# Kernel tuning notes

Measured on AMD Instinct MI355X. Metric: run time of the kernel, lower is better.

Reference implementation:

```python
import jax, jax.numpy as jnp
import numpy as np

N, E, H, NH = 50000, 800000, 128, 4
D = H // NH
EPS = 1e-5


def _ln(x, g, b):
    m = jnp.mean(x, axis=-1, keepdims=True)
    v = jnp.mean((x - m) ** 2, axis=-1, keepdims=True)
    return (x - m) * jax.lax.rsqrt(v + EPS) * g + b


def setup_inputs() -> dict:
    key = jax.random.key(0)
    ks = jax.random.split(key, 16)

    def lin(k, fi, fo):
        w = jax.random.normal(k, (fi, fo), jnp.float32) * (1.0 / np.sqrt(fi))
        return w, jnp.zeros((fo,), jnp.float32)

    h = jax.random.normal(ks[0], (N, H), jnp.float32)
    e = jax.random.normal(ks[1], (E, H), jnp.float32)
    src = jax.random.randint(ks[2], (E,), 0, N, jnp.int32)
    dst = jax.random.randint(ks[3], (E,), 0, N, jnp.int32)

    Wq, bq = lin(ks[4], H, H)
    Wk, bk = lin(ks[5], 2 * H, H)
    Wv, bv = lin(ks[6], 2 * H, H)
    Wn1, bn1 = lin(ks[7], H, H)
    Wn2, bn2 = lin(ks[8], H, H)
    We1, be1 = lin(ks[9], 3 * H, H)
    We2, be2 = lin(ks[10], H, H)
    gh = jnp.ones((H,), jnp.float32)
    bh = jnp.zeros((H,), jnp.float32)
    ge = jnp.ones((H,), jnp.float32)
    be = jnp.zeros((H,), jnp.float32)

    return dict(h=h, e=e, src=src, dst=dst, Wq=Wq, bq=bq, Wk=Wk, bk=bk,
                Wv=Wv, bv=bv, Wn1=Wn1, bn1=bn1, Wn2=Wn2, bn2=bn2,
                We1=We1, be1=be1, We2=We2, be2=be2, gh=gh, bh=bh, ge=ge, be=be)


def reference(h, e, src, dst, Wq, bq, Wk, bk, Wv, bv, Wn1, bn1, Wn2, bn2,
              We1, be1, We2, be2, gh, bh, ge, be):
    # gather src node features onto edges, concat with edge features: [E, 2H]
    m = jnp.concatenate([h[src], e], axis=-1)
    Q = (h @ Wq + bq).reshape(N, NH, D)
    K = (m @ Wk + bk).reshape(E, NH, D)
    V = (m @ Wv + bv).reshape(E, NH, D)

    # per-edge multihead attention score against destination query: [E, NH]
    s = jnp.sum(Q[dst] * K, axis=-1) / np.sqrt(D).astype(np.float32)

    # destination-grouped (segment) softmax per head
    smax = jax.ops.segment_max(s, dst, num_segments=N)  # [N, NH]
    a = jnp.exp(s - smax[dst])
    denom = jax.ops.segment_sum(a, dst, num_segments=N)  # [N, NH]
    a = a / denom[dst]

    # weighted scatter-sum of values back to destination nodes
    msg = V * a[..., None]  # [E, NH, D]
    h_agg = jax.ops.segment_sum(msg, dst, num_segments=N).reshape(N, H)

    # node MLP update (dropout = identity in eval) + residual + LayerNorm
    h_new = jax.nn.relu(jax.nn.relu(h_agg @ Wn1 + bn1) @ Wn2 + bn2)
    h_out = _ln(h + h_new, gh, bh)

    # edge MLP update on [src_h, dst_h, e] + residual + LayerNorm
    me = jnp.concatenate([h_out[src], h_out[dst], e], axis=-1)  # [E, 3H]
    e_new = jax.nn.relu(jax.nn.relu(me @ We1 + be1) @ We2 + be2)
    e_out = _ln(e + e_new, ge, be)
    return h_out, e_out
```

## Files before the change

### kernel.cpp

```cpp
#include <hip/hip_runtime.h>
#include <hip/hip_bf16.h>

#define NN 50000
#define EE 800000
#define HH 128

typedef __attribute__((ext_vector_type(8))) short bf16x8;
typedef __attribute__((ext_vector_type(4))) float f32x4;

__device__ inline unsigned short f2bf(float f) {
    union { float f; unsigned u; } v; v.f = f;
    unsigned r = v.u + 0x7FFF + ((v.u >> 16) & 1);
    return (unsigned short)(r >> 16);
}

__global__ __launch_bounds__(256) void hist_k(const int* __restrict__ dst, int* __restrict__ cnt) {
    int i = blockIdx.x * 256 + threadIdx.x;
    if (i < EE) atomicAdd(&cnt[dst[i]], 1);
}

__global__ __launch_bounds__(256) void blocksum_k(const int* __restrict__ cnt, int* __restrict__ bsum) {
    __shared__ int sm[256];
    int i = blockIdx.x * 256 + threadIdx.x;
    sm[threadIdx.x] = (i < NN) ? cnt[i] : 0;
    __syncthreads();
    for (int s = 128; s > 0; s >>= 1) {
        if (threadIdx.x < s) sm[threadIdx.x] += sm[threadIdx.x + s];
        __syncthreads();
    }
    if (threadIdx.x == 0) bsum[blockIdx.x] = sm[0];
}

__global__ __launch_bounds__(256) void scanb_k(int* __restrict__ bsum, int nb) {
    __shared__ int sm[256];
    int t = threadIdx.x;
    sm[t] = (t < nb) ? bsum[t] : 0;
    __syncthreads();
    for (int d = 1; d < 256; d <<= 1) {
        int v = (t >= d) ? sm[t - d] : 0;
        __syncthreads();
        sm[t] += v;
        __syncthreads();
    }
    if (t < nb) bsum[t] = sm[t];
}

__global__ __launch_bounds__(256) void offsets_k(const int* __restrict__ cnt, const int* __restrict__ bsum,
                                                 int* __restrict__ offsets, int* __restrict__ cursor) {
    __shared__ int sm[256];
    int b = blockIdx.x, t = threadIdx.x;
    int i = b * 256 + t;
    int c = (i < NN) ? cnt[i] : 0;
    sm[t] = c;
    __syncthreads();
    for (int d = 1; d < 256; d <<= 1) {
        int v = (t >= d) ? sm[t - d] : 0;
        __syncthreads();
        sm[t] += v;
        __syncthreads();
    }
    int incl = sm[t];
    int base = (b == 0) ? 0 : bsum[b - 1];
    int off = base + incl - c;
    if (i < NN) { offsets[i] = off; cursor[i] = off; }
    if (i == NN - 1) offsets[NN] = off + c;
}

__global__ __launch_bounds__(256) void fill_k(const int* __restrict__ dst, int* __restrict__ cursor,
                                              int* __restrict__ eids) {
    int i = blockIdx.x * 256 + threadIdx.x;
    if (i < EE) { int p = atomicAdd(&cursor[dst[i]], 1); eids[p] = i; }
}

__global__ __launch_bounds__(256) void wprep_k(const float* __restrict__ W, unsigned short* __restrict__ out,
                                               int fi, int fo, int n_off, int out_ld) {
    int i = blockIdx.x * 256 + threadIdx.x;
    if (i >= fi * fo) return;
    int n = i / fi, k = i - n * fi;
    out[(size_t)(n_off + n) * out_ld + k] = f2bf(W[(size_t)k * fo + n]);
}

__global__ __launch_bounds__(256) void cvt_k(const float* __restrict__ in, unsigned short* __restrict__ out,
                                             long n8) {
    long i = (long)blockIdx.x * 256 + threadIdx.x;
    if (i >= n8) return;
    const float4* p = (const float4*)in + i * 2;
    float4 a = p[0], b = p[1];
    bf16x8 o = {(short)f2bf(a.x), (short)f2bf(a.y), (short)f2bf(a.z), (short)f2bf(a.w),
                (short)f2bf(b.x), (short)f2bf(b.y), (short)f2bf(b.z), (short)f2bf(b.w)};
    *((bf16x8*)out + i) = o;
}

template <int G, int NCW, int RT, int MODE>
__global__ __launch_bounds__(512, 2) void mm4_k(
    const unsigned short* __restrict__ A0, const int* __restrict__ idx0,
    const unsigned short* __restrict__ A1, const int* __restrict__ idx1,
    const unsigned short* __restrict__ A2, const int* __restrict__ idx2,
    const unsigned short* __restrict__ Wt, const float* __restrict__ bias,
    int M,
    float* __restrict__ Cf, unsigned short* __restrict__ Cb, int out_ld)
{
    constexpr int RW = 8 / NCW;
    constexpr int ROWS = RW * RT * 16;
    constexpr int Ktot = G * 128;
    constexpr int SI = ROWS / 32;
    __shared__ unsigned short Asl[G * ROWS * 128];

    const int t = threadIdx.x;
    const int wid = t >> 6, lane = t & 63;
    const int lr = lane & 15, lk = lane >> 4;
    const int colw = (NCW == 8) ? wid : (wid & 3);
    const int roww = (NCW == 8) ? 0 : (wid >> 2);
    const int col0 = colw << 5;
    const int tbase = blockIdx.x * ROWS;

    const unsigned short* As[3] = {A0, A1, A2};
    const int* igs[3] = {idx0, idx1, idx2};

    #pragma unroll
    for (int g = 0; g < G; ++g) {
        const unsigned short* Ag = As[g];
        const int* ig = igs[g];
        #pragma unroll
        for (int i = 0; i < SI; ++i) {
            int rl = ((i * 8 + wid) << 2) + (lane >> 4);
            int gr = tbase + rl; if (gr >= M) gr = M - 1;
            int rid = ig ? ig[gr] : gr;
            const unsigned short* src = Ag + (size_t)rid * HH + (((lane & 15) ^ (rl & 7)) << 3);
            unsigned short* dst = &Asl[(g * ROWS + ((i * 8 + wid) << 2)) << 7];
            __builtin_amdgcn_global_load_lds((const __attribute__((address_space(1))) void*)src,
                                             (__attribute__((address_space(3))) void*)dst, 16, 0, 0);
        }
    }

    f32x4 acc[RT][2];
    #pragma unroll
    for (int tt = 0; tt < RT; ++tt) { acc[tt][0] = (f32x4){0,0,0,0}; acc[tt][1] = (f32x4){0,0,0,0}; }

    __syncthreads();

    #pragma unroll
    for (int g = 0; g < G; ++g) {
        bf16x8 b[4][2];
        #pragma unroll
        for (int s = 0; s < 4; ++s)
            #pragma unroll
            for (int c = 0; c < 2; ++c)
                b[s][c] = *(const bf16x8*)(Wt + (size_t)(col0 + (c << 4) + lr) * Ktot + (g << 7) + (s << 5) + (lk << 3));

        #pragma unroll
        for (int tt = 0; tt < RT; ++tt) {
            const int tl = (tt * RW + roww) << 4;
            bf16x8 a[4];
            #pragma unroll
            for (int s = 0; s < 4; ++s) {
                const int c16 = ((s << 2) + lk) ^ (lr & 7);
                a[s] = *(const bf16x8*)&Asl[((g * ROWS + tl + lr) << 7) + (c16 << 3)];
            }
            #pragma unroll
            for (int s = 0; s < 4; ++s) {
                acc[tt][0] = __builtin_amdgcn_mfma_f32_16x16x32_bf16(a[s], b[s][0], acc[tt][0], 0, 0, 0);
                acc[tt][1] = __builtin_amdgcn_mfma_f32_16x16x32_bf16(a[s], b[s][1], acc[tt][1], 0, 0, 0);
            }
        }
    }

    float bias2[2] = {bias[col0 + lr], bias[col0 + 16 + lr]};
    #pragma unroll
    for (int tt = 0; tt < RT; ++tt) {
        #pragma unroll
        for (int rr = 0; rr < 4; ++rr) {
            int row = tbase + ((tt * RW + roww) << 4) + (lk << 2) + rr;
            if (row >= M) continue;
            #pragma unroll
            for (int c = 0; c < 2; ++c) {
                float v = acc[tt][c][rr] + bias2[c];
                if (MODE == 1 || MODE == 4) v = fmaxf(v, 0.f);
                size_t o = (size_t)row * out_ld + col0 + (c << 4) + lr;
                if (MODE == 0 || MODE == 1) Cf[o] = v;
                else Cb[o] = f2bf(v);
            }
        }
    }
}

template <int G, int RT>
__global__ __launch_bounds__(512, 2) void mlp_k(
    const unsigned short* __restrict__ A0, const int* __restrict__ idx0,
    const unsigned short* __restrict__ A1, const int* __restrict__ idx1,
    const unsigned short* __restrict__ A2, const int* __restrict__ idx2,
    const unsigned short* __restrict__ W1t, const float* __restrict__ b1,
    const unsigned short* __restrict__ W2t, const float* __restrict__ b2,
    int M,
    float* __restrict__ Cf, unsigned short* __restrict__ Cb2,
    const float* __restrict__ resid, const float* __restrict__ gamma, const float* __restrict__ beta)
{
    constexpr int RW = 2, NCW = 4;
    constexpr int ROWS = RW * RT * 16;
    constexpr int K1 = G * 128;
    constexpr int SI = ROWS / 32;
    __shared__ unsigned short Asl[G * ROWS * 128];
    __shared__ float lnbuf[RT * 32 * 8];

    const int t = threadIdx.x;
    const int wid = t >> 6, lane = t & 63;
    const int lr = lane & 15, lk = lane >> 4;
    const int colw = wid & 3, roww = wid >> 2;
    const int col0 = colw << 5;
    const int tbase = blockIdx.x * ROWS;

    const unsigned short* As[3] = {A0, A1, A2};
    const int* igs[3] = {idx0, idx1, idx2};

    #pragma unroll
    for (int g = 0; g < G; ++g) {
        const unsigned short* Ag = As[g];
        const int* ig = igs[g];
        #pragma unroll
        for (int i = 0; i < SI; ++i) {
            int rl = ((i * 8 + wid) << 2) + (lane >> 4);
            int gr = tbase + rl; if (gr >= M) gr = M - 1;
            int rid = ig ? ig[gr] : gr;
            const unsigned short* src = Ag + (size_t)rid * HH + (((lane & 15) ^ (rl & 7)) << 3);
            unsigned short* dst = &Asl[(g * ROWS + ((i * 8 + wid) << 2)) << 7];
            __builtin_amdgcn_global_load_lds((const __attribute__((address_space(1))) void*)src,
                                             (__attribute__((address_space(3))) void*)dst, 16, 0, 0);
        }
    }

    f32x4 acc[RT][2];
    #pragma unroll
    for (int tt = 0; tt < RT; ++tt) { acc[tt][0] = (f32x4){0,0,0,0}; acc[tt][1] = (f32x4){0,0,0,0}; }

    __syncthreads();

    #pragma unroll
    for (int g = 0; g < G; ++g) {
        bf16x8 b[4][2];
        #pragma unroll
        for (int s = 0; s < 4; ++s)
            #pragma unroll
            for (int c = 0; c < 2; ++c)
                b[s][c] = *(const bf16x8*)(W1t + (size_t)(col0 + (c << 4) + lr) * K1 + (g << 7) + (s << 5) + (lk << 3));

        #pragma unroll
        for (int tt = 0; tt < RT; ++tt) {
            const int tl = (tt * RW + roww) << 4;
            bf16x8 a[4];
            #pragma unroll
            for (int s = 0; s < 4; ++s) {
                const int c16 = ((s << 2) + lk) ^ (lr & 7);
                a[s] = *(const bf16x8*)&Asl[((g * ROWS + tl + lr) << 7) + (c16 << 3)];
            }
            #pragma unroll
            for (int s = 0; s < 4; ++s) {
                acc[tt][0] = __builtin_amdgcn_mfma_f32_16x16x32_bf16(a[s], b[s][0], acc[tt][0], 0, 0, 0);
                acc[tt][1] = __builtin_amdgcn_mfma_f32_16x16x32_bf16(a[s], b[s][1], acc[tt][1], 0, 0, 0);
            }
        }
    }

    __syncthreads();

    {
        float b1c[2] = {b1[col0 + lr], b1[col0 + 16 + lr]};
        #pragma unroll
        for (int tt = 0; tt < RT; ++tt) {
            #pragma unroll
            for (int rr = 0; rr < 4; ++rr) {
                int rowl = ((tt * RW + roww) << 4) + (lk << 2) + rr;
                #pragma unroll
                for (int c = 0; c < 2; ++c) {
                    int col = col0 + (c << 4) + lr;
                    int chunk = (col >> 3) ^ (rowl & 7);
                    Asl[(rowl << 7) + (chunk << 3) + (col & 7)] =
                        f2bf(fmaxf(acc[tt][c][rr] + b1c[c], 0.f));
                }
            }
        }
    }

    __syncthreads();

    f32x4 acc2[RT][2];
    #pragma unroll
    for (int tt = 0; tt < RT; ++tt) { acc2[tt][0] = (f32x4){0,0,0,0}; acc2[tt][1] = (f32x4){0,0,0,0}; }

    {
        bf16x8 b[4][2];
        #pragma unroll
        for (int s = 0; s < 4; ++s)
            #pragma unroll
            for (int c = 0; c < 2; ++c)
                b[s][c] = *(const bf16x8*)(W2t + (size_t)(col0 + (c << 4) + lr) * 128 + (s << 5) + (lk << 3));

        #pragma unroll
        for (int tt = 0; tt < RT; ++tt) {
            const int tl = (tt * RW + roww) << 4;
            bf16x8 a[4];
            #pragma unroll
            for (int s = 0; s < 4; ++s) {
                const int c16 = ((s << 2) + lk) ^ (lr & 7);
                a[s] = *(const bf16x8*)&Asl[((tl + lr) << 7) + (c16 << 3)];
            }
            #pragma unroll
            for (int s = 0; s < 4; ++s) {
                acc2[tt][0] = __builtin_amdgcn_mfma_f32_16x16x32_bf16(a[s], b[s][0], acc2[tt][0], 0, 0, 0);
                acc2[tt][1] = __builtin_amdgcn_mfma_f32_16x16x32_bf16(a[s], b[s][1], acc2[tt][1], 0, 0, 0);
            }
        }
    }

    float b2c[2] = {b2[col0 + lr], b2[col0 + 16 + lr]};
    float g2[2] = {gamma[col0 + lr], gamma[col0 + 16 + lr]};
    float be2[2] = {beta[col0 + lr], beta[col0 + 16 + lr]};

    #pragma unroll
    for (int tt = 0; tt < RT; ++tt) {
        #pragma unroll
        for (int rr = 0; rr < 4; ++rr) {
            int row = tbase + ((tt * RW + roww) << 4) + (lk << 2) + rr;
            int rowc = (row < M) ? row : M - 1;
            float sum = 0.f, sq = 0.f;
            #pragma unroll
            for (int c = 0; c < 2; ++c) {
                float v = fmaxf(acc2[tt][c][rr] + b2c[c], 0.f);
                v += resid[(size_t)rowc * HH + col0 + (c << 4) + lr];
                acc2[tt][c][rr] = v;
                sum += v; sq += v * v;
            }
            sum += __shfl_xor(sum, 1); sq += __shfl_xor(sq, 1);
            sum += __shfl_xor(sum, 2); sq += __shfl_xor(sq, 2);
            sum += __shfl_xor(sum, 4); sq += __shfl_xor(sq, 4);
            sum += __shfl_xor(sum, 8); sq += __shfl_xor(sq, 8);
            if (lr == 0) {
                int rls = (roww << 4) + (lk << 2) + rr;
                lnbuf[((tt * 32 + rls) << 3) + (colw << 1) + 0] = sum;
                lnbuf[((tt * 32 + rls) << 3) + (colw << 1) + 1] = sq;
            }
        }
    }
    __syncthreads();
    #pragma unroll
    for (int tt = 0; tt < RT; ++tt) {
        #pragma unroll
        for (int rr = 0; rr < 4; ++rr) {
            int rls = (roww << 4) + (lk << 2) + rr;
            float s4 = 0.f, q4 = 0.f;
            #pragma unroll
            for (int cw = 0; cw < 4; ++cw) {
                s4 += lnbuf[((tt * 32 + rls) << 3) + (cw << 1) + 0];
                q4 += lnbuf[((tt * 32 + rls) << 3) + (cw << 1) + 1];
            }
            const float mean = s4 * (1.f / 128.f);
            const float var = q4 * (1.f / 128.f) - mean * mean;
            const float rs = rsqrtf(var + 1e-5f);
            int row = tbase + ((tt * RW + roww) << 4) + (lk << 2) + rr;
            if (row < M) {
                #pragma unroll
                for (int c = 0; c < 2; ++c) {
                    float o = (acc2[tt][c][rr] - mean) * rs * g2[c] + be2[c];
                    size_t idx = (size_t)row * HH + col0 + (c << 4) + lr;
                    Cf[idx] = o;
                    if (Cb2) Cb2[idx] = f2bf(o);
                }
            }
        }
    }
}

template <int RT>
__global__ __launch_bounds__(512, 2) void kv_k(
    const unsigned short* __restrict__ hbf, const int* __restrict__ src,
    const unsigned short* __restrict__ ebf,
    const unsigned short* __restrict__ Wt, const float* __restrict__ bias,
    const float* __restrict__ Q, const int* __restrict__ dst,
    int M, unsigned short* __restrict__ V, float* __restrict__ sbuf)
{
    constexpr int ROWS = RT * 16;
    constexpr int Ktot = 256;
    constexpr int SI = ROWS / 32;
    __shared__ unsigned short Asl[2 * ROWS * 128];

    const int t = threadIdx.x;
    const int wid = t >> 6, lane = t & 63;
    const int lr = lane & 15, lk = lane >> 4;
    const int col0 = wid << 5;
    const int tbase = blockIdx.x * ROWS;

    int dstid[RT][4];
    if (wid < 4) {
        #pragma unroll
        for (int tt = 0; tt < RT; ++tt)
            #pragma unroll
            for (int rr = 0; rr < 4; ++rr) {
                int row = tbase + (tt << 4) + (lk << 2) + rr;
                dstid[tt][rr] = dst[(row < M) ? row : M - 1];
            }
    }

    #pragma unroll
    for (int g = 0; g < 2; ++g) {
        const unsigned short* Ag = g ? ebf : hbf;
        #pragma unroll
        for (int i = 0; i < SI; ++i) {
            int rl = ((i * 8 + wid) << 2) + (lane >> 4);
            int gr = tbase + rl; if (gr >= M) gr = M - 1;
            int rid = g ? gr : src[gr];
            const unsigned short* srcp = Ag + (size_t)rid * HH + (((lane & 15) ^ (rl & 7)) << 3);
            unsigned short* dstp = &Asl[(g * ROWS + ((i * 8 + wid) << 2)) << 7];
            __builtin_amdgcn_global_load_lds((const __attribute__((address_space(1))) void*)srcp,
                                             (__attribute__((address_space(3))) void*)dstp, 16, 0, 0);
        }
    }

    f32x4 acc[RT][2];
    #pragma unroll
    for (int tt = 0; tt < RT; ++tt) { acc[tt][0] = (f32x4){0,0,0,0}; acc[tt][1] = (f32x4){0,0,0,0}; }

    __syncthreads();

    #pragma unroll
    for (int g = 0; g < 2; ++g) {
        bf16x8 b[4][2];
        #pragma unroll
        for (int s = 0; s < 4; ++s)
            #pragma unroll
            for (int c = 0; c < 2; ++c)
                b[s][c] = *(const bf16x8*)(Wt + (size_t)(col0 + (c << 4) + lr) * Ktot + (g << 7) + (s << 5) + (lk << 3));

        #pragma unroll
        for (int tt = 0; tt < RT; ++tt) {
            bf16x8 a[4];
            #pragma unroll
            for (int s = 0; s < 4; ++s) {
                const int c16 = ((s << 2) + lk) ^ (lr & 7);
                a[s] = *(const bf16x8*)&Asl[((g * ROWS + (tt << 4) + lr) << 7) + (c16 << 3)];
            }
            #pragma unroll
            for (int s = 0; s < 4; ++s) {
                acc[tt][0] = __builtin_amdgcn_mfma_f32_16x16x32_bf16(a[s], b[s][0], acc[tt][0], 0, 0, 0);
                acc[tt][1] = __builtin_amdgcn_mfma_f32_16x16x32_bf16(a[s], b[s][1], acc[tt][1], 0, 0, 0);
            }
        }
    }

    float bias2[2] = {bias[col0 + lr], bias[col0 + 16 + lr]};

    if (wid < 4) {
        #pragma unroll
        for (int tt = 0; tt < RT; ++tt) {
            #pragma unroll
            for (int rr = 0; rr < 4; ++rr) {
                int row = tbase + (tt << 4) + (lk << 2) + rr;
                int d = dstid[tt][rr];
                float q0 = Q[(size_t)d * HH + col0 + lr];
                float q1 = Q[(size_t)d * HH + col0 + 16 + lr];
                float p = (acc[tt][0][rr] + bias2[0]) * q0 + (acc[tt][1][rr] + bias2[1]) * q1;
                p += __shfl_xor(p, 1); p += __shfl_xor(p, 2);
                p += __shfl_xor(p, 4); p += __shfl_xor(p, 8);
                if (lr == 0 && row < M)
                    sbuf[(size_t)row * 4 + wid] = p * 0.17677669529663687f;
            }
        }
    } else {
        #pragma unroll
        for (int tt = 0; tt < RT; ++tt) {
            #pragma unroll
            for (int rr = 0; rr < 4; ++rr) {
                int row = tbase + (tt << 4) + (lk << 2) + rr;
                if (row >= M) continue;
                #pragma unroll
                for (int c = 0; c < 2; ++c)
                    V[(size_t)row * HH + (col0 - 128) + (c << 4) + lr] = f2bf(acc[tt][c][rr] + bias2[c]);
            }
        }
    }
}

__global__ __launch_bounds__(256) void agg_k(const __hip_bfloat16* __restrict__ Vb,
                                             const float* __restrict__ s,
                                             const int* __restrict__ offsets,
                                             const int* __restrict__ eids,
                                             unsigned short* __restrict__ hagg)
{
    const int t = threadIdx.x;
    const int n = blockIdx.x * 4 + (t >> 6);
    if (n >= NN) return;
    const int lane = t & 63;
    const int c0 = lane, c1 = lane + 64;
    const int h0 = lane >> 5, h1 = h0 + 2;
    const int o0 = offsets[n], o1 = offsets[n + 1];
    float m0 = -1e30f, m1 = -1e30f, d0 = 0.f, d1 = 0.f, a0 = 0.f, a1 = 0.f;
    for (int j = o0; j < o1; ++j) {
        const int e = eids[j];
        const float s0 = s[(size_t)e * 4 + h0];
        const float s1 = s[(size_t)e * 4 + h1];
        const float v0 = __bfloat162float(Vb[(size_t)e * HH + c0]);
        const float v1 = __bfloat162float(Vb[(size_t)e * HH + c1]);
        float nm = fmaxf(m0, s0);
        float sc = __expf(m0 - nm);
        float w  = __expf(s0 - nm);
        d0 = d0 * sc + w; a0 = a0 * sc + w * v0; m0 = nm;
        nm = fmaxf(m1, s1);
        sc = __expf(m1 - nm);
        w  = __expf(s1 - nm);
        d1 = d1 * sc + w; a1 = a1 * sc + w * v1; m1 = nm;
    }
    const bool any = (o1 > o0);
    hagg[(size_t)n * HH + c0] = any ? f2bf(a0 / d0) : 0;
    hagg[(size_t)n * HH + c1] = any ? f2bf(a1 / d1) : 0;
}

extern "C" void kernel_launch(void* const* d_in, const int* in_sizes, int n_in,
                              void* d_out, int out_size, void* d_ws, size_t ws_size,
                              hipStream_t stream)
{
    const float* h   = (const float*)d_in[0];
    const float* e   = (const float*)d_in[1];
    const int*   src = (const int*)d_in[2];
    const int*   dst = (const int*)d_in[3];
    const float* Wq  = (const float*)d_in[4];
    const float* bq  = (const float*)d_in[5];
    const float* Wk  = (const float*)d_in[6];
    const float* bk  = (const float*)d_in[7];
    const float* Wv  = (const float*)d_in[8];
    const float* bv  = (const float*)d_in[9];
    const float* Wn1 = (const float*)d_in[10];
    const float* bn1 = (const float*)d_in[11];
    const float* Wn2 = (const float*)d_in[12];
    const float* bn2 = (const float*)d_in[13];
    const float* We1 = (const float*)d_in[14];
    const float* be1 = (const float*)d_in[15];
    const float* We2 = (const float*)d_in[16];
    const float* be2 = (const float*)d_in[17];
    const float* gh  = (const float*)d_in[18];
    const float* bh  = (const float*)d_in[19];
    const float* ge  = (const float*)d_in[20];
    const float* be_ = (const float*)d_in[21];
    (void)in_sizes; (void)n_in; (void)out_size; (void)ws_size;

    float* h_out = (float*)d_out;
    float* e_out = (float*)d_out + (size_t)NN * HH;

    char* ws = (char*)d_ws;
    size_t off = 0;
    auto carve = [&](size_t bytes) { void* p = ws + off; off += (bytes + 255) & ~(size_t)255; return p; };
    unsigned short* Vbuf = (unsigned short*)carve((size_t)EE * HH * 2);
    unsigned short* ebf = (unsigned short*)carve((size_t)EE * HH * 2);
    float* Q      = (float*)carve((size_t)NN * HH * 4);
    float* sbuf   = (float*)carve((size_t)EE * 4 * 4);
    unsigned short* hagg = (unsigned short*)carve((size_t)NN * HH * 2);
    unsigned short* hobf = (unsigned short*)carve((size_t)NN * HH * 2);
    unsigned short* hbf  = (unsigned short*)carve((size_t)NN * HH * 2);
    int* cursor   = (int*)carve((size_t)NN * 4);
    int* offsets  = (int*)carve((size_t)(NN + 1) * 4);
    int* bsum     = (int*)carve(256 * 4);
    int* eids     = (int*)carve((size_t)EE * 4);
    unsigned short* Wq_s  = (unsigned short*)carve(128 * 128 * 2);
    unsigned short* Wkv_s = (unsigned short*)carve(256 * 256 * 2);
    unsigned short* Wn1_s = (unsigned short*)carve(128 * 128 * 2);
    unsigned short* Wn2_s = (unsigned short*)carve(128 * 128 * 2);
    unsigned short* We1_s = (unsigned short*)carve(128 * 384 * 2);
    unsigned short* We2_s = (unsigned short*)carve(128 * 128 * 2);
    float* b_kv   = (float*)carve(256 * 4);

    const int nb = (NN + 255) / 256;

    wprep_k<<<(128 * 128 + 255) / 256, 256, 0, stream>>>(Wq,  Wq_s,  128, 128, 0, 128);
    wprep_k<<<(256 * 128 + 255) / 256, 256, 0, stream>>>(Wk,  Wkv_s, 256, 128, 0, 256);
    wprep_k<<<(256 * 128 + 255) / 256, 256, 0, stream>>>(Wv,  Wkv_s, 256, 128, 128, 256);
    wprep_k<<<(128 * 128 + 255) / 256, 256, 0, stream>>>(Wn1, Wn1_s, 128, 128, 0, 128);
    wprep_k<<<(128 * 128 + 255) / 256, 256, 0, stream>>>(Wn2, Wn2_s, 128, 128, 0, 128);
    wprep_k<<<(384 * 128 + 255) / 256, 256, 0, stream>>>(We1, We1_s, 384, 128, 0, 384);
    wprep_k<<<(128 * 128 + 255) / 256, 256, 0, stream>>>(We2, We2_s, 128, 128, 0, 128);
    hipMemcpyAsync(b_kv,       bk, 128 * 4, hipMemcpyDeviceToDevice, stream);
    hipMemcpyAsync(b_kv + 128, bv, 128 * 4, hipMemcpyDeviceToDevice, stream);

    cvt_k<<<(NN * HH / 8 + 255) / 256, 256, 0, stream>>>(h, hbf, (long)NN * HH / 8);
    cvt_k<<<(EE * HH / 8 + 255) / 256, 256, 0, stream>>>(e, ebf, (long)EE * HH / 8);

    hipMemsetAsync(cursor, 0, (size_t)NN * 4, stream);
    hist_k<<<(EE + 255) / 256, 256, 0, stream>>>(dst, cursor);
    blocksum_k<<<nb, 256, 0, stream>>>(cursor, bsum);
    scanb_k<<<1, 256, 0, stream>>>(bsum, nb);
    offsets_k<<<nb, 256, 0, stream>>>(cursor, bsum, offsets, cursor);
    fill_k<<<(EE + 255) / 256, 256, 0, stream>>>(dst, cursor, eids);

    mm4_k<1, 4, 4, 0><<<(NN + 127) / 128, 512, 0, stream>>>(
        hbf, nullptr, nullptr, nullptr, nullptr, nullptr,
        Wq_s, bq, NN, Q, nullptr, 128);

    kv_k<4><<<EE / 64, 512, 0, stream>>>(
        hbf, src, ebf, Wkv_s, b_kv, Q, dst, EE, Vbuf, sbuf);

    agg_k<<<(NN + 3) / 4, 256, 0, stream>>>((const __hip_bfloat16*)Vbuf, sbuf, offsets, eids, hagg);

    mlp_k<1, 4><<<(NN + 127) / 128, 512, 0, stream>>>(
        hagg, nullptr, nullptr, nullptr, nullptr, nullptr,
        Wn1_s, bn1, Wn2_s, bn2, NN, h_out, hobf, h, gh, bh);

    mlp_k<3, 2><<<EE / 64, 512, 0, stream>>>(
        hobf, src, hobf, dst, ebf, nullptr,
        We1_s, be1, We2_s, be2, EE, e_out, nullptr, e, ge, be_);
}
```

Measured before the change: 1.340 ms.

## Make edge GEMM kernels persistent with double-buffered async LDS staging

Replaces the one-tile-per-block KV projection and MLP kernels with multi-tile loops that prefetch the next tile's gathered rows into a second LDS buffer while computing the current tile. Waits use explicit vmcnt and lgkmcnt counts, and residual loads are hoisted before the compute. The MLP tile shrinks to 32 rows with a separate intermediate buffer. The goal is to hide gather latency behind MFMA work, at the cost of fragile hand-set wait counts and fewer blocks in flight.

```diff
diff --git a/kernel.cpp b/kernel.cpp
--- a/kernel.cpp
+++ b/kernel.cpp
@@ -13,6 +13,19 @@
     unsigned r = v.u + 0x7FFF + ((v.u >> 16) & 1);
     return (unsigned short)(r >> 16);
 }
+
+template <int N> __device__ __forceinline__ void wait_vmcnt() {
+    static_assert(N == 4 || N == 9 || N == 11, "");
+    if constexpr (N == 4)  asm volatile("s_waitcnt vmcnt(4)" ::: "memory");
+    if constexpr (N == 9)  asm volatile("s_waitcnt vmcnt(9)" ::: "memory");
+    if constexpr (N == 11) asm volatile("s_waitcnt vmcnt(11)" ::: "memory");
+    __builtin_amdgcn_sched_barrier(0);
+}
+__device__ __forceinline__ void wait_lgkm0() {
+    asm volatile("s_waitcnt lgkmcnt(0)" ::: "memory");
+    __builtin_amdgcn_sched_barrier(0);
+}
+__device__ __forceinline__ void membar() { asm volatile("" ::: "memory"); }
 
 __global__ __launch_bounds__(256) void hist_k(const int* __restrict__ dst, int* __restrict__ cnt) {
     int i = blockIdx.x * 256 + threadIdx.x;
@@ -94,8 +107,6 @@
 template <int G, int NCW, int RT, int MODE>
 __global__ __launch_bounds__(512, 2) void mm4_k(
     const unsigned short* __restrict__ A0, const int* __restrict__ idx0,
-    const unsigned short* __restrict__ A1, const int* __restrict__ idx1,
-    const unsigned short* __restrict__ A2, const int* __restrict__ idx2,
     const unsigned short* __restrict__ Wt, const float* __restrict__ bias,
     int M,
     float* __restrict__ Cf, unsigned short* __restrict__ Cb, int out_ld)
@@ -109,24 +120,19 @@
     const int t = threadIdx.x;
     const int wid = t >> 6, lane = t & 63;
     const int lr = lane & 15, lk = lane >> 4;
-    const int colw = (NCW == 8) ? wid : (wid & 3);
-    const int roww = (NCW == 8) ? 0 : (wid >> 2);
+    const int colw = wid & 3;
+    const int roww = wid >> 2;
     const int col0 = colw << 5;
     const int tbase = blockIdx.x * ROWS;
 
-    const unsigned short* As[3] = {A0, A1, A2};
-    const int* igs[3] = {idx0, idx1, idx2};
-
     #pragma unroll
     for (int g = 0; g < G; ++g) {
-        const unsigned short* Ag = As[g];
-        const int* ig = igs[g];
         #pragma unroll
         for (int i = 0; i < SI; ++i) {
             int rl = ((i * 8 + wid) << 2) + (lane >> 4);
             int gr = tbase + rl; if (gr >= M) gr = M - 1;
-            int rid = ig ? ig[gr] : gr;
-            const unsigned short* src = Ag + (size_t)rid * HH + (((lane & 15) ^ (rl & 7)) << 3);
+            int rid = idx0 ? idx0[gr] : gr;
+            const unsigned short* src = A0 + (size_t)rid * HH + (((lane & 15) ^ (rl & 7)) << 3);
             unsigned short* dst = &Asl[(g * ROWS + ((i * 8 + wid) << 2)) << 7];
             __builtin_amdgcn_global_load_lds((const __attribute__((address_space(1))) void*)src,
                                              (__attribute__((address_space(3))) void*)dst, 16, 0, 0);
@@ -175,7 +181,7 @@
             #pragma unroll
             for (int c = 0; c < 2; ++c) {
                 float v = acc[tt][c][rr] + bias2[c];
-                if (MODE == 1 || MODE == 4) v = fmaxf(v, 0.f);
+                if (MODE == 1) v = fmaxf(v, 0.f);
                 size_t o = (size_t)row * out_ld + col0 + (c << 4) + lr;
                 if (MODE == 0 || MODE == 1) Cf[o] = v;
                 else Cb[o] = f2bf(v);
@@ -184,149 +190,263 @@
     }
 }
 
-template <int G, int RT>
-__global__ __launch_bounds__(512, 2) void mlp_k(
+template <int TPB>
+__global__ __launch_bounds__(512, 2) void kvp_k(
+    const unsigned short* __restrict__ hbf, const int* __restrict__ src,
+    const unsigned short* __restrict__ ebf,
+    const unsigned short* __restrict__ Wt, const float* __restrict__ bias,
+    const float* __restrict__ Q, const int* __restrict__ dst,
+    int M, int ntiles, unsigned short* __restrict__ V, float* __restrict__ sbuf)
+{
+    __shared__ unsigned short Abuf[2][2 * 64 * 128];
+
+    const int t = threadIdx.x;
+    const int wid = t >> 6, lane = t & 63;
+    const int lr = lane & 15, lk = lane >> 4;
+    const int col0 = wid << 5;
+    const int tb = blockIdx.x * TPB;
+
+    auto stage = [&](int tile, int buf) {
+        const int base = tile * 64;
+        #pragma unroll
+        for (int g = 0; g < 2; ++g) {
+            const unsigned short* Ag = g ? ebf : hbf;
+            #pragma unroll
+            for (int i = 0; i < 2; ++i) {
+                int rl = i * 32 + (t >> 4);
+                int gr = base + rl; if (gr >= M) gr = M - 1;
+                int rid = g ? gr : src[gr];
+                const unsigned short* sp = Ag + (size_t)rid * HH + (((t & 15) ^ (rl & 7)) << 3);
+                unsigned short* dp = &Abuf[buf][((g * 64 + rl) << 7) + ((t & 15) << 3)];
+                __builtin_amdgcn_global_load_lds((const __attribute__((address_space(1))) void*)sp,
+                                                 (__attribute__((address_space(3))) void*)dp, 16, 0, 0);
+            }
+        }
+    };
+
+    float bias2[2] = {bias[col0 + lr], bias[col0 + 16 + lr]};
+
+    stage(min(tb, ntiles - 1), 0);
+
+    for (int tt = 0; tt < TPB; ++tt) {
+        const int cur = tt & 1;
+        const int tile = min(tb + tt, ntiles - 1);
+        const int rbase = tile * 64;
+
+        if (tt + 1 < TPB) stage(min(tb + tt + 1, ntiles - 1), cur ^ 1);
+
+        int dstid[4][4];
+        if (wid < 4) {
+            #pragma unroll
+            for (int t4 = 0; t4 < 4; ++t4)
+                #pragma unroll
+                for (int rr = 0; rr < 4; ++rr) {
+                    int row = rbase + (t4 << 4) + (lk << 2) + rr;
+                    dstid[t4][rr] = dst[(row < M) ? row : M - 1];
+                }
+        }
+
+        wait_vmcnt<4>();
+        __builtin_amdgcn_s_barrier();
+
+        f32x4 acc[4][2];
+        #pragma unroll
+        for (int t4 = 0; t4 < 4; ++t4) { acc[t4][0] = (f32x4){0,0,0,0}; acc[t4][1] = (f32x4){0,0,0,0}; }
+
+        #pragma unroll
+        for (int g = 0; g < 2; ++g) {
+            bf16x8 b[4][2];
+            #pragma unroll
+            for (int s = 0; s < 4; ++s)
+                #pragma unroll
+                for (int c = 0; c < 2; ++c)
+                    b[s][c] = *(const bf16x8*)(Wt + (size_t)(col0 + (c << 4) + lr) * 256 + (g << 7) + (s << 5) + (lk << 3));
+
+            #pragma unroll
+            for (int t4 = 0; t4 < 4; ++t4) {
+                bf16x8 a[4];
+                #pragma unroll
+                for (int s = 0; s < 4; ++s) {
+                    const int c16 = ((s << 2) + lk) ^ (lr & 7);
+                    a[s] = *(const bf16x8*)&Abuf[cur][((g * 64 + (t4 << 4) + lr) << 7) + (c16 << 3)];
+                }
+                #pragma unroll
+                for (int s = 0; s < 4; ++s) {
+                    acc[t4][0] = __builtin_amdgcn_mfma_f32_16x16x32_bf16(a[s], b[s][0], acc[t4][0], 0, 0, 0);
+                    acc[t4][1] = __builtin_amdgcn_mfma_f32_16x16x32_bf16(a[s], b[s][1], acc[t4][1], 0, 0, 0);
+                }
+            }
+        }
+
+        if (wid < 4) {
+            #pragma unroll
+            for (int t4 = 0; t4 < 4; ++t4) {
+                #pragma unroll
+                for (int rr = 0; rr < 4; ++rr) {
+                    int row = rbase + (t4 << 4) + (lk << 2) + rr;
+                    int d = dstid[t4][rr];
+                    float q0 = Q[(size_t)d * HH + col0 + lr];
+                    float q1 = Q[(size_t)d * HH + col0 + 16 + lr];
+                    float p = (acc[t4][0][rr] + bias2[0]) * q0 + (acc[t4][1][rr] + bias2[1]) * q1;
+                    p += __shfl_xor(p, 1); p += __shfl_xor(p, 2);
+                    p += __shfl_xor(p, 4); p += __shfl_xor(p, 8);
+                    if (lr == 0 && row < M)
+                        sbuf[(size_t)row * 4 + wid] = p * 0.17677669529663687f;
+                }
+            }
+        } else {
+            #pragma unroll
+            for (int t4 = 0; t4 < 4; ++t4) {
+                #pragma unroll
+                for (int rr = 0; rr < 4; ++rr) {
+                    int row = rbase + (t4 << 4) + (lk << 2) + rr;
+                    if (row >= M) continue;
+                    #pragma unroll
+                    for (int c = 0; c < 2; ++c)
+                        V[(size_t)row * HH + (col0 - 128) + (c << 4) + lr] = f2bf(acc[t4][c][rr] + bias2[c]);
+                }
+            }
+        }
+
+        membar();
+        __builtin_amdgcn_s_barrier();
+    }
+}
+
+template <int G, int TPB>
+__global__ __launch_bounds__(512, 2) void mlpp_k(
     const unsigned short* __restrict__ A0, const int* __restrict__ idx0,
     const unsigned short* __restrict__ A1, const int* __restrict__ idx1,
     const unsigned short* __restrict__ A2, const int* __restrict__ idx2,
     const unsigned short* __restrict__ W1t, const float* __restrict__ b1,
     const unsigned short* __restrict__ W2t, const float* __restrict__ b2,
-    int M,
+    int M, int ntiles,
     float* __restrict__ Cf, unsigned short* __restrict__ Cb2,
     const float* __restrict__ resid, const float* __restrict__ gamma, const float* __restrict__ beta)
 {
-    constexpr int RW = 2, NCW = 4;
-    constexpr int ROWS = RW * RT * 16;
     constexpr int K1 = G * 128;
-    constexpr int SI = ROWS / 32;
-    __shared__ unsigned short Asl[G * ROWS * 128];
-    __shared__ float lnbuf[RT * 32 * 8];
+    __shared__ unsigned short Abuf[2][G * 32 * 128];
+    __shared__ unsigned short tbuf[32 * 128];
+    __shared__ float lnbuf[32 * 8];
 
     const int t = threadIdx.x;
     const int wid = t >> 6, lane = t & 63;
     const int lr = lane & 15, lk = lane >> 4;
-    const int colw = wid & 3, roww = wid >> 2;
-    const int col0 = colw << 5;
-    const int tbase = blockIdx.x * ROWS;
+    const int cw = wid & 3, rg = wid >> 2;
+    const int col0 = cw << 5;
+    const int tb = blockIdx.x * TPB;
 
     const unsigned short* As[3] = {A0, A1, A2};
     const int* igs[3] = {idx0, idx1, idx2};
 
-    #pragma unroll
-    for (int g = 0; g < G; ++g) {
-        const unsigned short* Ag = As[g];
-        const int* ig = igs[g];
-        #pragma unroll
-        for (int i = 0; i < SI; ++i) {
-            int rl = ((i * 8 + wid) << 2) + (lane >> 4);
-            int gr = tbase + rl; if (gr >= M) gr = M - 1;
+    auto stage = [&](int tile, int buf) {
+        const int base = tile * 32;
+        #pragma unroll
+        for (int g = 0; g < G; ++g) {
+            const unsigned short* Ag = As[g];
+            const int* ig = igs[g];
+            int rl = t >> 4;
+            int gr = base + rl; if (gr >= M) gr = M - 1;
             int rid = ig ? ig[gr] : gr;
-            const unsigned short* src = Ag + (size_t)rid * HH + (((lane & 15) ^ (rl & 7)) << 3);
-            unsigned short* dst = &Asl[(g * ROWS + ((i * 8 + wid) << 2)) << 7];
-            __builtin_amdgcn_global_load_lds((const __attribute__((address_space(1))) void*)src,
-                                             (__attribute__((address_space(3))) void*)dst, 16, 0, 0);
-        }
-    }
-
-    f32x4 acc[RT][2];
-    #pragma unroll
-    for (int tt = 0; tt < RT; ++tt) { acc[tt][0] = (f32x4){0,0,0,0}; acc[tt][1] = (f32x4){0,0,0,0}; }
-
-    __syncthreads();
-
-    #pragma unroll
-    for (int g = 0; g < G; ++g) {
-        bf16x8 b[4][2];
-        #pragma unroll
-        for (int s = 0; s < 4; ++s)
+            const unsigned short* sp = Ag + (size_t)rid * HH + (((t & 15) ^ (rl & 7)) << 3);
+            unsigned short* dp = &Abuf[buf][((g * 32 + rl) << 7) + ((t & 15) << 3)];
+            __builtin_amdgcn_global_load_lds((const __attribute__((address_space(1))) void*)sp,
+                                             (__attribute__((address_space(3))) void*)dp, 16, 0, 0);
+        }
+    };
+
+    float b1c[2] = {b1[col0 + lr], b1[col0 + 16 + lr]};
+    float b2c[2] = {b2[col0 + lr], b2[col0 + 16 + lr]};
+    float g2[2]  = {gamma[col0 + lr], gamma[col0 + 16 + lr]};
+    float be2[2] = {beta[col0 + lr], beta[col0 + 16 + lr]};
+
+    stage(min(tb, ntiles - 1), 0);
+
+    for (int tt = 0; tt < TPB; ++tt) {
+        const int cur = tt & 1;
+        const int tile = min(tb + tt, ntiles - 1);
+        const int rbase = tile * 32;
+
+        if (tt + 1 < TPB) stage(min(tb + tt + 1, ntiles - 1), cur ^ 1);
+
+        float rp[4][2];
+        #pragma unroll
+        for (int rr = 0; rr < 4; ++rr) {
+            int row = rbase + (rg << 4) + (lk << 2) + rr;
+            int rowc = (row < M) ? row : M - 1;
             #pragma unroll
             for (int c = 0; c < 2; ++c)
-                b[s][c] = *(const bf16x8*)(W1t + (size_t)(col0 + (c << 4) + lr) * K1 + (g << 7) + (s << 5) + (lk << 3));
-
-        #pragma unroll
-        for (int tt = 0; tt < RT; ++tt) {
-            const int tl = (tt * RW + roww) << 4;
+                rp[rr][c] = resid[(size_t)rowc * HH + col0 + (c << 4) + lr];
+        }
+
+        wait_vmcnt<(G == 3) ? 11 : 9>();
+        __builtin_amdgcn_s_barrier();
+
+        f32x4 acc[2] = {(f32x4){0,0,0,0}, (f32x4){0,0,0,0}};
+        #pragma unroll
+        for (int g = 0; g < G; ++g) {
+            bf16x8 b[4][2];
+            #pragma unroll
+            for (int s = 0; s < 4; ++s)
+                #pragma unroll
+                for (int c = 0; c < 2; ++c)
+                    b[s][c] = *(const bf16x8*)(W1t + (size_t)(col0 + (c << 4) + lr) * K1 + (g << 7) + (s << 5) + (lk << 3));
             bf16x8 a[4];
             #pragma unroll
             for (int s = 0; s < 4; ++s) {
                 const int c16 = ((s << 2) + lk) ^ (lr & 7);
-                a[s] = *(const bf16x8*)&Asl[((g * ROWS + tl + lr) << 7) + (c16 << 3)];
+                a[s] = *(const bf16x8*)&Abuf[cur][((g * 32 + (rg << 4) + lr) << 7) + (c16 << 3)];
             }
             #pragma unroll
             for (int s = 0; s < 4; ++s) {
-                acc[tt][0] = __builtin_amdgcn_mfma_f32_16x16x32_bf16(a[s], b[s][0], acc[tt][0], 0, 0, 0);
-                acc[tt][1] = __builtin_amdgcn_mfma_f32_16x16x32_bf16(a[s], b[s][1], acc[tt][1], 0, 0, 0);
-            }
-        }
-    }
-
-    __syncthreads();
-
-    {
-        float b1c[2] = {b1[col0 + lr], b1[col0 + 16 + lr]};
-        #pragma unroll
-        for (int tt = 0; tt < RT; ++tt) {
-            #pragma unroll
-            for (int rr = 0; rr < 4; ++rr) {
-                int rowl = ((tt * RW + roww) << 4) + (lk << 2) + rr;
-                #pragma unroll
-                for (int c = 0; c < 2; ++c) {
-                    int col = col0 + (c << 4) + lr;
-                    int chunk = (col >> 3) ^ (rowl & 7);
-                    Asl[(rowl << 7) + (chunk << 3) + (col & 7)] =
-                        f2bf(fmaxf(acc[tt][c][rr] + b1c[c], 0.f));
-                }
-            }
-        }
-    }
-
-    __syncthreads();
-
-    f32x4 acc2[RT][2];
-    #pragma unroll
-    for (int tt = 0; tt < RT; ++tt) { acc2[tt][0] = (f32x4){0,0,0,0}; acc2[tt][1] = (f32x4){0,0,0,0}; }
-
-    {
-        bf16x8 b[4][2];
-        #pragma unroll
-        for (int s = 0; s < 4; ++s)
-            #pragma unroll
-            for (int c = 0; c < 2; ++c)
-                b[s][c] = *(const bf16x8*)(W2t + (size_t)(col0 + (c << 4) + lr) * 128 + (s << 5) + (lk << 3));
-
-        #pragma unroll
-        for (int tt = 0; tt < RT; ++tt) {
-            const int tl = (tt * RW + roww) << 4;
+                acc[0] = __builtin_amdgcn_mfma_f32_16x16x32_bf16(a[s], b[s][0], acc[0], 0, 0, 0);
+                acc[1] = __builtin_amdgcn_mfma_f32_16x16x32_bf16(a[s], b[s][1], acc[1], 0, 0, 0);
+            }
+        }
+
+        #pragma unroll
+        for (int rr = 0; rr < 4; ++rr) {
+            int rowl = (rg << 4) + (lk << 2) + rr;
+            #pragma unroll
+            for (int c = 0; c < 2; ++c) {
+                int col = col0 + (c << 4) + lr;
+                int chunk = (col >> 3) ^ (rowl & 7);
+                tbuf[(rowl << 7) + (chunk << 3) + (col & 7)] =
+                    f2bf(fmaxf(acc[c][rr] + b1c[c], 0.f));
+            }
+        }
+        wait_lgkm0();
+        __builtin_amdgcn_s_barrier();
+
+        f32x4 acc2[2] = {(f32x4){0,0,0,0}, (f32x4){0,0,0,0}};
+        {
+            bf16x8 b[4][2];
+            #pragma unroll
+            for (int s = 0; s < 4; ++s)
+                #pragma unroll
+                for (int c = 0; c < 2; ++c)
+                    b[s][c] = *(const bf16x8*)(W2t + (size_t)(col0 + (c << 4) + lr) * 128 + (s << 5) + (lk << 3));
             bf16x8 a[4];
             #pragma unroll
             for (int s = 0; s < 4; ++s) {
                 const int c16 = ((s << 2) + lk) ^ (lr & 7);
-                a[s] = *(const bf16x8*)&Asl[((tl + lr) << 7) + (c16 << 3)];
+                a[s] = *(const bf16x8*)&tbuf[(((rg << 4) + lr) << 7) + (c16 << 3)];
             }
             #pragma unroll
             for (int s = 0; s < 4; ++s) {
-                acc2[tt][0] = __builtin_amdgcn_mfma_f32_16x16x32_bf16(a[s], b[s][0], acc2[tt][0], 0, 0, 0);
-                acc2[tt][1] = __builtin_amdgcn_mfma_f32_16x16x32_bf16(a[s], b[s][1], acc2[tt][1], 0, 0, 0);
-            }
-        }
-    }
-
-    float b2c[2] = {b2[col0 + lr], b2[col0 + 16 + lr]};
-    float g2[2] = {gamma[col0 + lr], gamma[col0 + 16 + lr]};
-    float be2[2] = {beta[col0 + lr], beta[col0 + 16 + lr]};
-
-    #pragma unroll
-    for (int tt = 0; tt < RT; ++tt) {
+                acc2[0] = __builtin_amdgcn_mfma_f32_16x16x32_bf16(a[s], b[s][0], acc2[0], 0, 0, 0);
+                acc2[1] = __builtin_amdgcn_mfma_f32_16x16x32_bf16(a[s], b[s][1], acc2[1], 0, 0, 0);
+            }
+        }
+
+        float xv[4][2];
         #pragma unroll
         for (int rr = 0; rr < 4; ++rr) {
-            int row = tbase + ((tt * RW + roww) << 4) + (lk << 2) + rr;
-            int rowc = (row < M) ? row : M - 1;
             float sum = 0.f, sq = 0.f;
             #pragma unroll
             for (int c = 0; c < 2; ++c) {
-                float v = fmaxf(acc2[tt][c][rr] + b2c[c], 0.f);
-                v += resid[(size_t)rowc * HH + col0 + (c << 4) + lr];
-                acc2[tt][c][rr] = v;
+                float v = fmaxf(acc2[c][rr] + b2c[c], 0.f) + rp[rr][c];
+                xv[rr][c] = v;
                 sum += v; sq += v * v;
             }
             sum += __shfl_xor(sum, 1); sq += __shfl_xor(sq, 1);
@@ -334,145 +454,35 @@
             sum += __shfl_xor(sum, 4); sq += __shfl_xor(sq, 4);
             sum += __shfl_xor(sum, 8); sq += __shfl_xor(sq, 8);
             if (lr == 0) {
-                int rls = (roww << 4) + (lk << 2) + rr;
-                lnbuf[((tt * 32 + rls) << 3) + (colw << 1) + 0] = sum;
-                lnbuf[((tt * 32 + rls) << 3) + (colw << 1) + 1] = sq;
-            }
-        }
-    }
-    __syncthreads();
-    #pragma unroll
-    for (int tt = 0; tt < RT; ++tt) {
+                int rowl = (rg << 4) + (lk << 2) + rr;
+                lnbuf[(rowl << 3) + (cw << 1) + 0] = sum;
+                lnbuf[(rowl << 3) + (cw << 1) + 1] = sq;
+            }
+        }
+        wait_lgkm0();
+        __builtin_amdgcn_s_barrier();
+
         #pragma unroll
         for (int rr = 0; rr < 4; ++rr) {
-            int rls = (roww << 4) + (lk << 2) + rr;
+            int rowl = (rg << 4) + (lk << 2) + rr;
             float s4 = 0.f, q4 = 0.f;
             #pragma unroll
-            for (int cw = 0; cw < 4; ++cw) {
-                s4 += lnbuf[((tt * 32 + rls) << 3) + (cw << 1) + 0];
-                q4 += lnbuf[((tt * 32 + rls) << 3) + (cw << 1) + 1];
+            for (int w4 = 0; w4 < 4; ++w4) {
+                s4 += lnbuf[(rowl << 3) + (w4 << 1) + 0];
+                q4 += lnbuf[(rowl << 3) + (w4 << 1) + 1];
             }
             const float mean = s4 * (1.f / 128.f);
             const float var = q4 * (1.f / 128.f) - mean * mean;
             const float rs = rsqrtf(var + 1e-5f);
-            int row = tbase + ((tt * RW + roww) << 4) + (lk << 2) + rr;
+            int row = rbase + rowl;
             if (row < M) {
                 #pragma unroll
                 for (int c = 0; c < 2; ++c) {
-                    float o = (acc2[tt][c][rr] - mean) * rs * g2[c] + be2[c];
+                    float o = (xv[rr][c] - mean) * rs * g2[c] + be2[c];
                     size_t idx = (size_t)row * HH + col0 + (c << 4) + lr;
                     Cf[idx] = o;
                     if (Cb2) Cb2[idx] = f2bf(o);
                 }
-            }
-        }
-    }
-}
-
-template <int RT>
-__global__ __launch_bounds__(512, 2) void kv_k(
-    const unsigned short* __restrict__ hbf, const int* __restrict__ src,
-    const unsigned short* __restrict__ ebf,
-    const unsigned short* __restrict__ Wt, const float* __restrict__ bias,
-    const float* __restrict__ Q, const int* __restrict__ dst,
-    int M, unsigned short* __restrict__ V, float* __restrict__ sbuf)
-{
-    constexpr int ROWS = RT * 16;
-    constexpr int Ktot = 256;
-    constexpr int SI = ROWS / 32;
-    __shared__ unsigned short Asl[2 * ROWS * 128];
-
-    const int t = threadIdx.x;
-    const int wid = t >> 6, lane = t & 63;
-    const int lr = lane & 15, lk = lane >> 4;
-    const int col0 = wid << 5;
-    const int tbase = blockIdx.x * ROWS;
-
-    int dstid[RT][4];
-    if (wid < 4) {
-        #pragma unroll
-        for (int tt = 0; tt < RT; ++tt)
-            #pragma unroll
-            for (int rr = 0; rr < 4; ++rr) {
-                int row = tbase + (tt << 4) + (lk << 2) + rr;
-                dstid[tt][rr] = dst[(row < M) ? row : M - 1];
-            }
-    }
-
-    #pragma unroll
-    for (int g = 0; g < 2; ++g) {
-        const unsigned short* Ag = g ? ebf : hbf;
-        #pragma unroll
-        for (int i = 0; i < SI; ++i) {
-            int rl = ((i * 8 + wid) << 2) + (lane >> 4);
-            int gr = tbase + rl; if (gr >= M) gr = M - 1;
-            int rid = g ? gr : src[gr];
-            const unsigned short* srcp = Ag + (size_t)rid * HH + (((lane & 15) ^ (rl & 7)) << 3);
-            unsigned short* dstp = &Asl[(g * ROWS + ((i * 8 + wid) << 2)) << 7];
-            __builtin_amdgcn_global_load_lds((const __attribute__((address_space(1))) void*)srcp,
-                                             (__attribute__((address_space(3))) void*)dstp, 16, 0, 0);
-        }
-    }
-
-    f32x4 acc[RT][2];
-    #pragma unroll
-    for (int tt = 0; tt < RT; ++tt) { acc[tt][0] = (f32x4){0,0,0,0}; acc[tt][1] = (f32x4){0,0,0,0}; }
-
-    __syncthreads();
-
-    #pragma unroll
-    for (int g = 0; g < 2; ++g) {
-        bf16x8 b[4][2];
-        #pragma unroll
-        for (int s = 0; s < 4; ++s)
-            #pragma unroll
-            for (int c = 0; c < 2; ++c)
-                b[s][c] = *(const bf16x8*)(Wt + (size_t)(col0 + (c << 4) + lr) * Ktot + (g << 7) + (s << 5) + (lk << 3));
-
-        #pragma unroll
-        for (int tt = 0; tt < RT; ++tt) {
-            bf16x8 a[4];
-            #pragma unroll
-            for (int s = 0; s < 4; ++s) {
-                const int c16 = ((s << 2) + lk) ^ (lr & 7);
-                a[s] = *(const bf16x8*)&Asl[((g * ROWS + (tt << 4) + lr) << 7) + (c16 << 3)];
-            }
-            #pragma unroll
-            for (int s = 0; s < 4; ++s) {
-                acc[tt][0] = __builtin_amdgcn_mfma_f32_16x16x32_bf16(a[s], b[s][0], acc[tt][0], 0, 0, 0);
-                acc[tt][1] = __builtin_amdgcn_mfma_f32_16x16x32_bf16(a[s], b[s][1], acc[tt][1], 0, 0, 0);
-            }
-        }
-    }
-
-    float bias2[2] = {bias[col0 + lr], bias[col0 + 16 + lr]};
-
-    if (wid < 4) {
-        #pragma unroll
-        for (int tt = 0; tt < RT; ++tt) {
-            #pragma unroll
-            for (int rr = 0; rr < 4; ++rr) {
-                int row = tbase + (tt << 4) + (lk << 2) + rr;
-                int d = dstid[tt][rr];
-                float q0 = Q[(size_t)d * HH + col0 + lr];
-                float q1 = Q[(size_t)d * HH + col0 + 16 + lr];
-                float p = (acc[tt][0][rr] + bias2[0]) * q0 + (acc[tt][1][rr] + bias2[1]) * q1;
-                p += __shfl_xor(p, 1); p += __shfl_xor(p, 2);
-                p += __shfl_xor(p, 4); p += __shfl_xor(p, 8);
-                if (lr == 0 && row < M)
-                    sbuf[(size_t)row * 4 + wid] = p * 0.17677669529663687f;
-            }
-        }
-    } else {
-        #pragma unroll
-        for (int tt = 0; tt < RT; ++tt) {
-            #pragma unroll
-            for (int rr = 0; rr < 4; ++rr) {
-                int row = tbase + (tt << 4) + (lk << 2) + rr;
-                if (row >= M) continue;
-                #pragma unroll
-                for (int c = 0; c < 2; ++c)
-                    V[(size_t)row * HH + (col0 - 128) + (c << 4) + lr] = f2bf(acc[tt][c][rr] + bias2[c]);
             }
         }
     }
@@ -588,19 +598,27 @@
     fill_k<<<(EE + 255) / 256, 256, 0, stream>>>(dst, cursor, eids);
 
     mm4_k<1, 4, 4, 0><<<(NN + 127) / 128, 512, 0, stream>>>(
-        hbf, nullptr, nullptr, nullptr, nullptr, nullptr,
-        Wq_s, bq, NN, Q, nullptr, 128);
-
-    kv_k<4><<<EE / 64, 512, 0, stream>>>(
-        hbf, src, ebf, Wkv_s, b_kv, Q, dst, EE, Vbuf, sbuf);
+        hbf, nullptr, Wq_s, bq, NN, Q, nullptr, 128);
+
+    {
+        const int ntiles = EE / 64;
+        kvp_k<10><<<(ntiles + 9) / 10, 512, 0, stream>>>(
+            hbf, src, ebf, Wkv_s, b_kv, Q, dst, EE, ntiles, Vbuf, sbuf);
+    }
 
     agg_k<<<(NN + 3) / 4, 256, 0, stream>>>((const __hip_bfloat16*)Vbuf, sbuf, offsets, eids, hagg);
 
-    mlp_k<1, 4><<<(NN + 127) / 128, 512, 0, stream>>>(
-        hagg, nullptr, nullptr, nullptr, nullptr, nullptr,
-        Wn1_s, bn1, Wn2_s, bn2, NN, h_out, hobf, h, gh, bh);
-
-    mlp_k<3, 2><<<EE / 64, 512, 0, stream>>>(
-        hobf, src, hobf, dst, ebf, nullptr,
-        We1_s, be1, We2_s, be2, EE, e_out, nullptr, e, ge, be_);
-}
+    {
+        const int ntiles = (NN + 31) / 32;
+        mlpp_k<1, 3><<<(ntiles + 2) / 3, 512, 0, stream>>>(
+            hagg, nullptr, nullptr, nullptr, nullptr, nullptr,
+            Wn1_s, bn1, Wn2_s, bn2, NN, ntiles, h_out, hobf, h, gh, bh);
+    }
+
+    {
+        const int ntiles = EE / 32;
+        mlpp_k<3, 10><<<(ntiles + 9) / 10, 512, 0, stream>>>(
+            hobf, src, hobf, dst, ebf, nullptr,
+            We1_s, be1, We2_s, be2, EE, ntiles, e_out, nullptr, e, ge, be_);
+    }
+}
```

Result: slower. 2.049 ms (+52.9%).

## Process edges in destination-sorted order so aggregation reads V and scores contiguously

Applied to the files above, without the earlier changes.

The fill kernel now also writes src and dst indices permuted into CSR (dst-sorted) order. The K/V projection kernel walks edges in that sorted order, gathering e rows through eids and h rows through the permuted src. It writes V and scores at sorted positions, so the aggregation kernel reads them contiguously instead of through eids. This replaces scattered per-edge gathers of V and scores in aggregation with a gather of e rows in the KV kernel, at the cost of two extra int arrays. Unused generality in mm4_k (extra operand slots, NCW==8 path, MODE 4) is also removed.

```diff
diff --git a/kernel.cpp b/kernel.cpp
--- a/kernel.cpp
+++ b/kernel.cpp
@@ -66,10 +66,17 @@
     if (i == NN - 1) offsets[NN] = off + c;
 }
 
-__global__ __launch_bounds__(256) void fill_k(const int* __restrict__ dst, int* __restrict__ cursor,
-                                              int* __restrict__ eids) {
+__global__ __launch_bounds__(256) void fill_k(const int* __restrict__ src, const int* __restrict__ dst,
+                                              int* __restrict__ cursor, int* __restrict__ eids,
+                                              int* __restrict__ srcc, int* __restrict__ dstc) {
     int i = blockIdx.x * 256 + threadIdx.x;
-    if (i < EE) { int p = atomicAdd(&cursor[dst[i]], 1); eids[p] = i; }
+    if (i < EE) {
+        int d = dst[i];
+        int p = atomicAdd(&cursor[d], 1);
+        eids[p] = i;
+        srcc[p] = src[i];
+        dstc[p] = d;
+    }
 }
 
 __global__ __launch_bounds__(256) void wprep_k(const float* __restrict__ W, unsigned short* __restrict__ out,
@@ -94,8 +101,6 @@
 template <int G, int NCW, int RT, int MODE>
 __global__ __launch_bounds__(512, 2) void mm4_k(
     const unsigned short* __restrict__ A0, const int* __restrict__ idx0,
-    const unsigned short* __restrict__ A1, const int* __restrict__ idx1,
-    const unsigned short* __restrict__ A2, const int* __restrict__ idx2,
     const unsigned short* __restrict__ Wt, const float* __restrict__ bias,
     int M,
     float* __restrict__ Cf, unsigned short* __restrict__ Cb, int out_ld)
@@ -109,24 +114,19 @@
     const int t = threadIdx.x;
     const int wid = t >> 6, lane = t & 63;
     const int lr = lane & 15, lk = lane >> 4;
-    const int colw = (NCW == 8) ? wid : (wid & 3);
-    const int roww = (NCW == 8) ? 0 : (wid >> 2);
+    const int colw = wid & 3;
+    const int roww = wid >> 2;
     const int col0 = colw << 5;
     const int tbase = blockIdx.x * ROWS;
 
-    const unsigned short* As[3] = {A0, A1, A2};
-    const int* igs[3] = {idx0, idx1, idx2};
-
     #pragma unroll
     for (int g = 0; g < G; ++g) {
-        const unsigned short* Ag = As[g];
-        const int* ig = igs[g];
         #pragma unroll
         for (int i = 0; i < SI; ++i) {
             int rl = ((i * 8 + wid) << 2) + (lane >> 4);
             int gr = tbase + rl; if (gr >= M) gr = M - 1;
-            int rid = ig ? ig[gr] : gr;
-            const unsigned short* src = Ag + (size_t)rid * HH + (((lane & 15) ^ (rl & 7)) << 3);
+            int rid = idx0 ? idx0[gr] : gr;
+            const unsigned short* src = A0 + (size_t)rid * HH + (((lane & 15) ^ (rl & 7)) << 3);
             unsigned short* dst = &Asl[(g * ROWS + ((i * 8 + wid) << 2)) << 7];
             __builtin_amdgcn_global_load_lds((const __attribute__((address_space(1))) void*)src,
                                              (__attribute__((address_space(3))) void*)dst, 16, 0, 0);
@@ -175,7 +175,7 @@
             #pragma unroll
             for (int c = 0; c < 2; ++c) {
                 float v = acc[tt][c][rr] + bias2[c];
-                if (MODE == 1 || MODE == 4) v = fmaxf(v, 0.f);
+                if (MODE == 1) v = fmaxf(v, 0.f);
                 size_t o = (size_t)row * out_ld + col0 + (c << 4) + lr;
                 if (MODE == 0 || MODE == 1) Cf[o] = v;
                 else Cb[o] = f2bf(v);
@@ -371,10 +371,10 @@
 
 template <int RT>
 __global__ __launch_bounds__(512, 2) void kv_k(
-    const unsigned short* __restrict__ hbf, const int* __restrict__ src,
-    const unsigned short* __restrict__ ebf,
+    const unsigned short* __restrict__ hbf, const int* __restrict__ srcc,
+    const int* __restrict__ eids, const unsigned short* __restrict__ ebf,
     const unsigned short* __restrict__ Wt, const float* __restrict__ bias,
-    const float* __restrict__ Q, const int* __restrict__ dst,
+    const float* __restrict__ Q, const int* __restrict__ dstc,
     int M, unsigned short* __restrict__ V, float* __restrict__ sbuf)
 {
     constexpr int ROWS = RT * 16;
@@ -395,18 +395,19 @@
             #pragma unroll
             for (int rr = 0; rr < 4; ++rr) {
                 int row = tbase + (tt << 4) + (lk << 2) + rr;
-                dstid[tt][rr] = dst[(row < M) ? row : M - 1];
+                dstid[tt][rr] = dstc[(row < M) ? row : M - 1];
             }
     }
 
     #pragma unroll
     for (int g = 0; g < 2; ++g) {
         const unsigned short* Ag = g ? ebf : hbf;
+        const int* ig = g ? eids : srcc;
         #pragma unroll
         for (int i = 0; i < SI; ++i) {
             int rl = ((i * 8 + wid) << 2) + (lane >> 4);
             int gr = tbase + rl; if (gr >= M) gr = M - 1;
-            int rid = g ? gr : src[gr];
+            int rid = ig[gr];
             const unsigned short* srcp = Ag + (size_t)rid * HH + (((lane & 15) ^ (rl & 7)) << 3);
             unsigned short* dstp = &Asl[(g * ROWS + ((i * 8 + wid) << 2)) << 7];
             __builtin_amdgcn_global_load_lds((const __attribute__((address_space(1))) void*)srcp,
@@ -481,7 +482,6 @@
 __global__ __launch_bounds__(256) void agg_k(const __hip_bfloat16* __restrict__ Vb,
                                              const float* __restrict__ s,
                                              const int* __restrict__ offsets,
-                                             const int* __restrict__ eids,
                                              unsigned short* __restrict__ hagg)
 {
     const int t = threadIdx.x;
@@ -493,11 +493,10 @@
     const int o0 = offsets[n], o1 = offsets[n + 1];
     float m0 = -1e30f, m1 = -1e30f, d0 = 0.f, d1 = 0.f, a0 = 0.f, a1 = 0.f;
     for (int j = o0; j < o1; ++j) {
-        const int e = eids[j];
-        const float s0 = s[(size_t)e * 4 + h0];
-        const float s1 = s[(size_t)e * 4 + h1];
-        const float v0 = __bfloat162float(Vb[(size_t)e * HH + c0]);
-        const float v1 = __bfloat162float(Vb[(size_t)e * HH + c1]);
+        const float s0 = s[(size_t)j * 4 + h0];
+        const float s1 = s[(size_t)j * 4 + h1];
+        const float v0 = __bfloat162float(Vb[(size_t)j * HH + c0]);
+        const float v1 = __bfloat162float(Vb[(size_t)j * HH + c1]);
         float nm = fmaxf(m0, s0);
         float sc = __expf(m0 - nm);
         float w  = __expf(s0 - nm);
@@ -557,6 +556,8 @@
     int* offsets  = (int*)carve((size_t)(NN + 1) * 4);
     int* bsum     = (int*)carve(256 * 4);
     int* eids     = (int*)carve((size_t)EE * 4);
+    int* srcc     = (int*)carve((size_t)EE * 4);
+    int* dstc     = (int*)carve((size_t)EE * 4);
     unsigned short* Wq_s  = (unsigned short*)carve(128 * 128 * 2);
     unsigned short* Wkv_s = (unsigned short*)carve(256 * 256 * 2);
     unsigned short* Wn1_s = (unsigned short*)carve(128 * 128 * 2);
@@ -585,16 +586,15 @@
     blocksum_k<<<nb, 256, 0, stream>>>(cursor, bsum);
     scanb_k<<<1, 256, 0, stream>>>(bsum, nb);
     offsets_k<<<nb, 256, 0, stream>>>(cursor, bsum, offsets, cursor);
-    fill_k<<<(EE + 255) / 256, 256, 0, stream>>>(dst, cursor, eids);
+    fill_k<<<(EE + 255) / 256, 256, 0, stream>>>(src, dst, cursor, eids, srcc, dstc);
 
     mm4_k<1, 4, 4, 0><<<(NN + 127) / 128, 512, 0, stream>>>(
-        hbf, nullptr, nullptr, nullptr, nullptr, nullptr,
-        Wq_s, bq, NN, Q, nullptr, 128);
+        hbf, nullptr, Wq_s, bq, NN, Q, nullptr, 128);
 
     kv_k<4><<<EE / 64, 512, 0, stream>>>(
-        hbf, src, ebf, Wkv_s, b_kv, Q, dst, EE, Vbuf, sbuf);
-
-    agg_k<<<(NN + 3) / 4, 256, 0, stream>>>((const __hip_bfloat16*)Vbuf, sbuf, offsets, eids, hagg);
+        hbf, srcc, eids, ebf, Wkv_s, b_kv, Q, dstc, EE, Vbuf, sbuf);
+
+    agg_k<<<(NN + 3) / 4, 256, 0, stream>>>((const __hip_bfloat16*)Vbuf, sbuf, offsets, hagg);
 
     mlp_k<1, 4><<<(NN + 127) / 128, 512, 0, stream>>>(
         hagg, nullptr, nullptr, nullptr, nullptr, nullptr,
```

Measured after the change: 1.278 ms. 4.7% less time.
